# Kernel tuning notes

Measured on AMD Instinct MI355X. Metric: run time of the kernel, lower is better.

The kernel has to match this reference:

```python
import jax, jax.numpy as jnp
import numpy as np

KH = KW = 16  # kernel height/width == stride (non-overlapping patches)
E = KH * KW   # Linear in/out features = 256


def setup_inputs() -> dict:
    key = jax.random.key(0)
    k1, k2, k3 = jax.random.split(key, 3)
    H = W = 8192
    data = jax.random.normal(k1, (H, W), dtype=jnp.float32)
    # nn.Linear(E, E): weight (out, in), bias (out,)
    weight = jax.random.normal(k2, (E, E), dtype=jnp.float32) / np.sqrt(E).astype(np.float32)
    bias = jax.random.normal(k3, (E,), dtype=jnp.float32) * 0.01
    return {"data": data, "weight": weight, "bias": bias}


def reference(data, weight, bias):
    # DummyConv forward: for each stride-aligned (16x16) patch,
    # flatten -> Linear(E,E) -> sum -> scalar written to output grid.
    H, W = data.shape
    gh, gw = H // KH, W // KW
    # im2col for non-overlapping patches via reshape/transpose: (gh*gw, E)
    patches = data.reshape(gh, KH, gw, KW).transpose(0, 2, 1, 3).reshape(gh * gw, E)
    # torch Linear: y = x @ W.T + b ; then sum over output features per patch
    y = patches @ weight.T + bias  # (P, E)
    out = jnp.sum(y, axis=-1).reshape(gh, gw)  # (512, 512)
    return out
```

## Files before the change

kernel.cpp:

```cpp
#include <hip/hip_runtime.h>

#define KH 16
#define KW 16
#define E  256

typedef float f32x4 __attribute__((ext_vector_type(4)));

__global__ __launch_bounds__(1024) void DummyConv_prep_kernel(
    const float* __restrict__ weight,
    const float* __restrict__ bias,
    float* __restrict__ ws) {
    __shared__ __align__(16) f32x4 red[1024];
    __shared__ float bred[4];

    const int t  = threadIdx.x;
    const int c4 = t & 63;
    const int j0 = t >> 6;

    f32x4 a = {0.f, 0.f, 0.f, 0.f};
    for (int j = j0; j < E; j += 16) {
        a += *reinterpret_cast<const f32x4*>(&weight[j * E + c4 * 4]);
    }
    red[t] = a;

    if (t < E) {
        float b = bias[t];
        b += __shfl_xor(b, 1);  b += __shfl_xor(b, 2);  b += __shfl_xor(b, 4);
        b += __shfl_xor(b, 8);  b += __shfl_xor(b, 16); b += __shfl_xor(b, 32);
        if ((t & 63) == 0) bred[t >> 6] = b;
    }
    __syncthreads();

    if (t < 64) {
        f32x4 s = {0.f, 0.f, 0.f, 0.f};
#pragma unroll
        for (int k = 0; k < 16; ++k) s += red[k * 64 + t];
        *reinterpret_cast<f32x4*>(&ws[t * 4]) = s;
        if (t == 0) ws[E] = bred[0] + bred[1] + bred[2] + bred[3];
    }
}

__global__ __launch_bounds__(256) void DummyConv_main_kernel(
    const float* __restrict__ data,
    const float* __restrict__ ws,
    float* __restrict__ out) {
    constexpr int W  = 8192;
    constexpr int GW = 512;

    __shared__ __align__(16) float wsum[E];
    __shared__ float bsum_s;
    __shared__ float partials[4][64];

    const int t = threadIdx.x;
    wsum[t] = ws[t];
    if (t == 0) bsum_s = ws[E];
    __syncthreads();

    const int tileX = blockIdx.x & 31;
    const int gq    = blockIdx.x >> 5;
    const long rowBase = (long)gq * 64;
    const int  colBase = tileX * 256;

    const int c4    = t & 63;
    const int rquad = t >> 6;
    const int pc    = c4 >> 2;
    const int wcol  = (t & 3) * 4;

    f32x4 wv[4];
#pragma unroll
    for (int p = 0; p < 4; ++p)
        wv[p] = *reinterpret_cast<const f32x4*>(&wsum[(rquad + p * 4) * KW + wcol]);

    float acc[4] = {0.f, 0.f, 0.f, 0.f};
#pragma unroll
    for (int pr = 0; pr < 4; ++pr) {
#pragma unroll
        for (int p = 0; p < 4; ++p) {
            const long r = rowBase + pr * 16 + rquad + p * 4;
            const f32x4 d = __builtin_nontemporal_load(
                reinterpret_cast<const f32x4*>(data + r * W + colBase + c4 * 4));
            acc[pr] += d.x * wv[p].x + d.y * wv[p].y + d.z * wv[p].z + d.w * wv[p].w;
        }
    }

#pragma unroll
    for (int pr = 0; pr < 4; ++pr) {
        float a = acc[pr];
        a += __shfl_xor(a, 1);
        a += __shfl_xor(a, 2);
        if ((t & 3) == 0) partials[pr][pc * 4 + rquad] = a;
    }
    __syncthreads();

    if (t < 64) {
        const int pr  = t >> 4;
        const int pcc = t & 15;
        const float s = partials[pr][pcc * 4 + 0] + partials[pr][pcc * 4 + 1] +
                        partials[pr][pcc * 4 + 2] + partials[pr][pcc * 4 + 3] + bsum_s;
        out[((long)gq * 4 + pr) * GW + tileX * 16 + pcc] = s;
    }
}

extern "C" void kernel_launch(void* const* d_in, const int* in_sizes, int n_in,
                              void* d_out, int out_size, void* d_ws, size_t ws_size,
                              hipStream_t stream) {
    const float* data   = (const float*)d_in[0];
    const float* weight = (const float*)d_in[1];
    const float* bias   = (const float*)d_in[2];
    float* out = (float*)d_out;
    float* ws  = (float*)d_ws;

    DummyConv_prep_kernel<<<1, 1024, 0, stream>>>(weight, bias, ws);

    DummyConv_main_kernel<<<4096, 256, 0, stream>>>(data, ws, out);
}
```

Measured before the change: 57.20 us.

## Assign one wavefront per patch row and drop shared memory and barriers

The main kernel is restructured so each 64-lane wavefront covers a single 16-row by 256-column strip (16 patches). It reads weight sums directly from global memory instead of staging them in LDS, and reduces with shuffles only. This removes the shared-memory partials, both __syncthreads barriers, and the 64-thread final reduction stage. Blocks become 512 threads across 2048 blocks, and per-wave memory-level parallelism is unchanged at 16 loads per lane.

```diff
diff --git a/kernel.cpp b/kernel.cpp
--- a/kernel.cpp
+++ b/kernel.cpp
@@ -40,65 +40,37 @@
     }
 }
 
-__global__ __launch_bounds__(256) void DummyConv_main_kernel(
+__global__ __launch_bounds__(512) void DummyConv_main_kernel(
     const float* __restrict__ data,
     const float* __restrict__ ws,
     float* __restrict__ out) {
     constexpr int W  = 8192;
     constexpr int GW = 512;
 
-    __shared__ __align__(16) float wsum[E];
-    __shared__ float bsum_s;
-    __shared__ float partials[4][64];
+    const int t    = threadIdx.x;
+    const int lane = t & 63;
+    const int wid  = blockIdx.x * 8 + (t >> 6);
+    const int sy   = wid >> 5;
+    const int sx   = wid & 31;
 
-    const int t = threadIdx.x;
-    wsum[t] = ws[t];
-    if (t == 0) bsum_s = ws[E];
-    __syncthreads();
+    const float bsum = ws[E];
+    const float* wbase = ws + (lane & 3) * 4;
+    const float* dbase = data + (long)sy * 16 * W + sx * 256 + lane * 4;
 
-    const int tileX = blockIdx.x & 31;
-    const int gq    = blockIdx.x >> 5;
-    const long rowBase = (long)gq * 64;
-    const int  colBase = tileX * 256;
-
-    const int c4    = t & 63;
-    const int rquad = t >> 6;
-    const int pc    = c4 >> 2;
-    const int wcol  = (t & 3) * 4;
-
-    f32x4 wv[4];
+    float acc = 0.f;
 #pragma unroll
-    for (int p = 0; p < 4; ++p)
-        wv[p] = *reinterpret_cast<const f32x4*>(&wsum[(rquad + p * 4) * KW + wcol]);
-
-    float acc[4] = {0.f, 0.f, 0.f, 0.f};
-#pragma unroll
-    for (int pr = 0; pr < 4; ++pr) {
-#pragma unroll
-        for (int p = 0; p < 4; ++p) {
-            const long r = rowBase + pr * 16 + rquad + p * 4;
-            const f32x4 d = __builtin_nontemporal_load(
-                reinterpret_cast<const f32x4*>(data + r * W + colBase + c4 * 4));
-            acc[pr] += d.x * wv[p].x + d.y * wv[p].y + d.z * wv[p].z + d.w * wv[p].w;
-        }
+    for (int rr = 0; rr < 16; ++rr) {
+        const f32x4 d = __builtin_nontemporal_load(
+            reinterpret_cast<const f32x4*>(dbase + rr * W));
+        const f32x4 w = *reinterpret_cast<const f32x4*>(wbase + rr * KW);
+        acc += d.x * w.x + d.y * w.y + d.z * w.z + d.w * w.w;
     }
 
-#pragma unroll
-    for (int pr = 0; pr < 4; ++pr) {
-        float a = acc[pr];
-        a += __shfl_xor(a, 1);
-        a += __shfl_xor(a, 2);
-        if ((t & 3) == 0) partials[pr][pc * 4 + rquad] = a;
-    }
-    __syncthreads();
-
-    if (t < 64) {
-        const int pr  = t >> 4;
-        const int pcc = t & 15;
-        const float s = partials[pr][pcc * 4 + 0] + partials[pr][pcc * 4 + 1] +
-                        partials[pr][pcc * 4 + 2] + partials[pr][pcc * 4 + 3] + bsum_s;
-        out[((long)gq * 4 + pr) * GW + tileX * 16 + pcc] = s;
-    }
+    acc += __shfl_xor(acc, 1);
+    acc += __shfl_xor(acc, 2);
+    const float v = __shfl(acc, (lane & 15) * 4);
+    if (lane < 16)
+        out[sy * GW + sx * 16 + lane] = v + bsum;
 }
 
 extern "C" void kernel_launch(void* const* d_in, const int* in_sizes, int n_in,
@@ -112,5 +84,5 @@
 
     DummyConv_prep_kernel<<<1, 1024, 0, stream>>>(weight, bias, ws);
 
-    DummyConv_main_kernel<<<4096, 256, 0, stream>>>(data, ws, out);
+    DummyConv_main_kernel<<<2048, 512, 0, stream>>>(data, ws, out);
 }
```

Measured after the change: 49.84 us. -12.9%, faster.
